# Optimization experiments

Measured on AMD Instinct MI355X. Metric: run time of the kernel, lower is better.

The kernel has to match this reference:

```python
import jax, jax.numpy as jnp
import numpy as np

B, S, D, H, FF = 4, 1024, 1024, 16, 4096
DH = D // H
EPS = 1e-5  # torch LayerNorm default


def _layernorm(x, g, b):
    m = jnp.mean(x, axis=-1, keepdims=True)
    v = jnp.mean((x - m) ** 2, axis=-1, keepdims=True)
    return (x - m) * jax.lax.rsqrt(v + EPS) * g + b


def setup_inputs() -> dict:
    key = jax.random.key(0)
    ks = jax.random.split(key, 8)
    init = lambda k, shape: jax.random.normal(k, shape, jnp.float32) * 0.02
    return {
        "x": jax.random.normal(ks[0], (B, S, D), jnp.float32),
        "Wq": init(ks[1], (D, D)), "bq": jnp.zeros((D,), jnp.float32),
        "Wk": init(ks[2], (D, D)), "bk": jnp.zeros((D,), jnp.float32),
        "Wv": init(ks[3], (D, D)), "bv": jnp.zeros((D,), jnp.float32),
        "Wo": init(ks[4], (D, D)), "bo": jnp.zeros((D,), jnp.float32),
        "ln1_g": jnp.ones((D,), jnp.float32), "ln1_b": jnp.zeros((D,), jnp.float32),
        "W1": init(ks[5], (D, FF)), "b1": jnp.zeros((FF,), jnp.float32),
        "W2": init(ks[6], (FF, D)), "b2": jnp.zeros((D,), jnp.float32),
        "ln2_g": jnp.ones((D,), jnp.float32), "ln2_b": jnp.zeros((D,), jnp.float32),
    }


def reference(x, Wq, bq, Wk, bk, Wv, bv, Wo, bo,
              ln1_g, ln1_b, W1, b1, W2, b2, ln2_g, ln2_b):
    Bx, Sx, _ = x.shape

    def heads(w, b):  # [B,S,D] -> [B,H,S,DH]
        return (x @ w + b).reshape(Bx, Sx, H, DH).transpose(0, 2, 1, 3)

    q, k, v = heads(Wq, bq), heads(Wk, bk), heads(Wv, bv)
    scores = jnp.einsum('bhqd,bhkd->bhqk', q, k) / jnp.sqrt(jnp.float32(DH))
    causal = jnp.tril(jnp.ones((Sx, Sx), bool))
    scores = jnp.where(causal[None, None], scores, jnp.float32(-1e9))
    attn = jax.nn.softmax(scores, axis=-1)           # [B,H,S,S]
    ctx = jnp.einsum('bhqk,bhkd->bqhd', attn, v).reshape(Bx, Sx, D)
    attn_out = ctx @ Wo + bo
    h = _layernorm(x + attn_out, ln1_g, ln1_b)
    ff = jax.nn.relu(h @ W1 + b1) @ W2 + b2
    y = _layernorm(h + ff, ln2_g, ln2_b)
    return (y, attn)
```

## Files before the change

kernel.cpp:

```cpp
#include <hip/hip_runtime.h>
#include <cstdint>


#define T_B 4
#define T_S 1024
#define T_D 1024
#define T_H 16
#define T_DH 64
#define T_FF 4096
#define T_TOK (T_B * T_S)

typedef __attribute__((ext_vector_type(8))) short bf16x8;
typedef __attribute__((ext_vector_type(4))) float f32x4;

__device__ __forceinline__ short f2bf(float f) {
  uint32_t u = __float_as_uint(f);
  u += 0x7FFFu + ((u >> 16) & 1u);
  return (short)(u >> 16);
}

__device__ __forceinline__ void async_copy16(void* lds, const void* g) {
  __builtin_amdgcn_global_load_lds(
      (__attribute__((address_space(1))) uint32_t*)(uintptr_t)g,
      (__attribute__((address_space(3))) uint32_t*)(uint32_t)(uintptr_t)lds,
      16, 0, 0);
}

__device__ __forceinline__ void mfma_loop_128x128(
    const short* __restrict__ A, int lda, const short* __restrict__ Bm, int ldb,
    int kLen, int m0, int n0, short* As, short* Bs, f32x4 acc[4][4]) {
  const int t = threadIdx.x;
  const int lane = t & 63, wid = t >> 6;
  const int wm = (wid >> 1) << 6, wn = (wid & 1) << 6;
  const int quad = lane >> 4, r16 = lane & 15;
  const int row0 = t >> 2;
  const int cb0 = (t & 3) << 4;

  const f32x4 zf = {0.f, 0.f, 0.f, 0.f};
#pragma unroll
  for (int i = 0; i < 4; ++i)
#pragma unroll
    for (int j = 0; j < 4; ++j) acc[i][j] = zf;

  for (int k0 = 0; k0 < kLen; k0 += 32) {
    __syncthreads();
    async_copy16((char*)As + (wid << 10),
                 (const char*)A + (((size_t)(m0 + row0) * lda + k0) << 1) + cb0);
    async_copy16((char*)As + 4096 + (wid << 10),
                 (const char*)A + (((size_t)(m0 + 64 + row0) * lda + k0) << 1) + cb0);
    async_copy16((char*)Bs + (wid << 10),
                 (const char*)Bm + (((size_t)(n0 + row0) * ldb + k0) << 1) + cb0);
    async_copy16((char*)Bs + 4096 + (wid << 10),
                 (const char*)Bm + (((size_t)(n0 + 64 + row0) * ldb + k0) << 1) + cb0);
    __syncthreads();
    bf16x8 av[4], bv[4];
#pragma unroll
    for (int i = 0; i < 4; ++i) {
      av[i] = *(const bf16x8*)(As + ((wm + i * 16 + r16) << 5) + (quad << 3));
      bv[i] = *(const bf16x8*)(Bs + ((wn + i * 16 + r16) << 5) + (quad << 3));
    }
#pragma unroll
    for (int mi = 0; mi < 4; ++mi)
#pragma unroll
      for (int ni = 0; ni < 4; ++ni)
        acc[mi][ni] = __builtin_amdgcn_mfma_f32_16x16x32_bf16(
            av[mi], bv[ni], acc[mi][ni], 0, 0, 0);
  }
}

template <int MODE>
__global__ __launch_bounds__(256) void gemm_dense(
    const short* __restrict__ A, const short* __restrict__ Bw, int K, int N,
    const float* __restrict__ bias0, const float* __restrict__ bias1,
    const float* __restrict__ bias2, short* __restrict__ outb0,
    short* __restrict__ outb1, short* __restrict__ outb2) {
  __shared__ __align__(16) short As[128 * 32];
  __shared__ __align__(16) short Bs[128 * 32];
  const int m0 = blockIdx.x << 7, n0 = blockIdx.y << 7;
  f32x4 acc[4][4];
  mfma_loop_128x128(A, K, Bw, K, K, m0, n0, As, Bs, acc);

  const int t = threadIdx.x;
  const int lane = t & 63, wid = t >> 6;
  const int wm = (wid >> 1) << 6, wn = (wid & 1) << 6;
  const int quad = lane >> 4, r16 = lane & 15;

  if constexpr (MODE == 0) {
    const int which = n0 >> 10;
    const float* bias = (which == 0) ? bias0 : (which == 1) ? bias1 : bias2;
#pragma unroll
    for (int mi = 0; mi < 4; ++mi) {
#pragma unroll
      for (int ni = 0; ni < 4; ++ni) {
        const int col = n0 + wn + ni * 16 + r16;
        const int c10 = col & 1023;
        const float bb = bias[c10];
        const int hh = c10 >> 6, dh = col & 63;
#pragma unroll
        for (int reg = 0; reg < 4; ++reg) {
          const int row = m0 + wm + mi * 16 + quad * 4 + reg;
          const int b = row >> 10, s = row & 1023;
          const short v = f2bf(acc[mi][ni][reg] + bb);
          if (which == 0)
            outb0[((((size_t)b * T_H + hh) * T_S) + s) * T_DH + dh] = v;
          else if (which == 1)
            outb1[((((size_t)b * T_H + hh) * T_S) + s) * T_DH + dh] = v;
          else
            outb2[(((size_t)b * T_H + hh) * T_DH + dh) * T_S + s] = v;
        }
      }
    }
  } else {
#pragma unroll
    for (int mi = 0; mi < 4; ++mi)
#pragma unroll
      for (int ni = 0; ni < 4; ++ni) {
        const int col = n0 + wn + ni * 16 + r16;
        const float bb = bias0[col];
#pragma unroll
        for (int reg = 0; reg < 4; ++reg) {
          const int row = m0 + wm + mi * 16 + quad * 4 + reg;
          outb0[(size_t)row * N + col] = f2bf(fmaxf(acc[mi][ni][reg] + bb, 0.f));
        }
      }
  }
}

__global__ __launch_bounds__(256) void gemm_splitk(
    const short* __restrict__ A, const short* __restrict__ Bw, int K, int N,
    int kc, float* __restrict__ outp) {
  __shared__ __align__(16) short As[128 * 32];
  __shared__ __align__(16) short Bs[128 * 32];
  const int m0 = blockIdx.x << 7, n0 = blockIdx.y << 7, z = blockIdx.z;
  f32x4 acc[4][4];
  mfma_loop_128x128(A + (size_t)z * kc, K, Bw + (size_t)z * kc, K, kc, m0, n0,
                    As, Bs, acc);
  float* o = outp + (size_t)z * T_TOK * N;
  const int t = threadIdx.x;
  const int lane = t & 63, wid = t >> 6;
  const int wm = (wid >> 1) << 6, wn = (wid & 1) << 6;
  const int quad = lane >> 4, r16 = lane & 15;
#pragma unroll
  for (int mi = 0; mi < 4; ++mi)
#pragma unroll
    for (int ni = 0; ni < 4; ++ni) {
      const int col = n0 + wn + ni * 16 + r16;
#pragma unroll
      for (int reg = 0; reg < 4; ++reg) {
        const int row = m0 + wm + mi * 16 + quad * 4 + reg;
        o[(size_t)row * N + col] = acc[mi][ni][reg];
      }
    }
}

__global__ __launch_bounds__(256) void attn_pass1(
    const short* __restrict__ qg, const short* __restrict__ kg,
    const short* __restrict__ vg, short* __restrict__ ctx,
    float* __restrict__ rsinv_g) {
  const int qb = blockIdx.x;
  const int bh = blockIdx.y;
  const int b = bh >> 4, h = bh & 15;
  const int m0 = qb << 7;
  __shared__ __align__(16) short Es[4 * 128 * 32];
  __shared__ float rsbuf[2][128];
  const int t = threadIdx.x;
  const int lane = t & 63, wid = t >> 6;
  const int quad = lane >> 4, r16 = lane & 15;
  const int wm = (wid >> 1) << 6, wn = (wid & 1) << 6;
  const int pvm = wid << 5;

  const short* Qbh = qg + (size_t)bh * T_S * T_DH;
  const short* Kbh = kg + (size_t)bh * T_S * T_DH;
  const short* Vbh = vg + (size_t)bh * T_DH * T_S;

  bf16x8 qf[4][2];
#pragma unroll
  for (int mi = 0; mi < 4; ++mi)
#pragma unroll
    for (int ksd = 0; ksd < 2; ++ksd)
      qf[mi][ksd] = *(const bf16x8*)(Qbh + (size_t)(m0 + wm + mi * 16 + r16) * T_DH +
                                     ksd * 32 + quad * 8);

  float rs[4][4];
#pragma unroll
  for (int i = 0; i < 4; ++i)
#pragma unroll
    for (int j = 0; j < 4; ++j) rs[i][j] = 0.f;
  const f32x4 zf = {0.f, 0.f, 0.f, 0.f};
  f32x4 accp[2][4];
#pragma unroll
  for (int i = 0; i < 2; ++i)
#pragma unroll
    for (int j = 0; j < 4; ++j) accp[i][j] = zf;

  for (int kt = 0; kt <= qb; ++kt) {
    f32x4 accs[4][4];
#pragma unroll
    for (int i = 0; i < 4; ++i)
#pragma unroll
      for (int j = 0; j < 4; ++j) accs[i][j] = zf;
#pragma unroll
    for (int ksd = 0; ksd < 2; ++ksd) {
      bf16x8 bv[4];
#pragma unroll
      for (int ni = 0; ni < 4; ++ni)
        bv[ni] = *(const bf16x8*)(Kbh + (size_t)(kt * 128 + wn + ni * 16 + r16) * T_DH +
                                  ksd * 32 + quad * 8);
#pragma unroll
      for (int mi = 0; mi < 4; ++mi)
#pragma unroll
        for (int ni = 0; ni < 4; ++ni)
          accs[mi][ni] = __builtin_amdgcn_mfma_f32_16x16x32_bf16(
              qf[mi][ksd], bv[ni], accs[mi][ni], 0, 0, 0);
    }
    __syncthreads();
    const bool diag = (kt == qb);
#pragma unroll
    for (int mi = 0; mi < 4; ++mi) {
#pragma unroll
      for (int ni = 0; ni < 4; ++ni) {
        const int cbase = wn + ni * 16;
        const int kse = cbase >> 5;
        const int sin = (cbase & 31) + r16;
        short* ep = Es + kse * 4096 + (wm + mi * 16 + quad * 4) * 32 + sin;
        const int colw = cbase + r16;
#pragma unroll
        for (int reg = 0; reg < 4; ++reg) {
          float e = __expf(accs[mi][ni][reg] * 0.125f);
          if (diag && colw > (wm + mi * 16 + quad * 4 + reg)) e = 0.f;
          ep[reg * 32] = f2bf(e);
          rs[mi][reg] += e;
        }
      }
    }
    __syncthreads();
#pragma unroll
    for (int ks = 0; ks < 4; ++ks) {
      bf16x8 av[2], bvv[4];
#pragma unroll
      for (int i = 0; i < 2; ++i)
        av[i] = *(const bf16x8*)(Es + ks * 4096 + (pvm + i * 16 + r16) * 32 + quad * 8);
#pragma unroll
      for (int ni = 0; ni < 4; ++ni)
        bvv[ni] = *(const bf16x8*)(Vbh + (size_t)(ni * 16 + r16) * T_S + kt * 128 +
                                   ks * 32 + quad * 8);
#pragma unroll
      for (int i = 0; i < 2; ++i)
#pragma unroll
        for (int ni = 0; ni < 4; ++ni)
          accp[i][ni] = __builtin_amdgcn_mfma_f32_16x16x32_bf16(av[i], bvv[ni],
                                                                accp[i][ni], 0, 0, 0);
    }
  }

#pragma unroll
  for (int mi = 0; mi < 4; ++mi)
#pragma unroll
    for (int reg = 0; reg < 4; ++reg) {
#pragma unroll
      for (int d = 1; d < 16; d <<= 1)
        rs[mi][reg] += __shfl_xor(rs[mi][reg], d, 64);
    }
  if (r16 == 0) {
#pragma unroll
    for (int mi = 0; mi < 4; ++mi)
#pragma unroll
      for (int reg = 0; reg < 4; ++reg)
        rsbuf[wid & 1][wm + mi * 16 + quad * 4 + reg] = rs[mi][reg];
  }
  __syncthreads();
  if (t < 128) {
    const float iv = 1.f / (rsbuf[0][t] + rsbuf[1][t]);
    rsbuf[0][t] = iv;
    rsinv_g[(size_t)bh * T_S + m0 + t] = iv;
  }
  __syncthreads();
#pragma unroll
  for (int i = 0; i < 2; ++i)
#pragma unroll
    for (int ni = 0; ni < 4; ++ni) {
#pragma unroll
      for (int reg = 0; reg < 4; ++reg) {
        const int row = pvm + i * 16 + quad * 4 + reg;
        const float iv = rsbuf[0][row];
        ctx[((size_t)b * T_S + m0 + row) * T_D + h * 64 + ni * 16 + r16] =
            f2bf(accp[i][ni][reg] * iv);
      }
    }
}

__global__ __launch_bounds__(256) void attn_pass2(
    const short* __restrict__ qg, const short* __restrict__ kg,
    const float* __restrict__ rsinv_g, float* __restrict__ attn) {
  const int qb = blockIdx.x, kt = blockIdx.y, bh = blockIdx.z;
  float* out = attn + ((size_t)bh * T_S + qb * 128) * T_S + kt * 128;
  const int t = threadIdx.x;
  if (kt > qb) {
    const float4 z4 = {0.f, 0.f, 0.f, 0.f};
#pragma unroll
    for (int j = 0; j < 16; ++j) {
      const int id = t + j * 256;
      ((float4*)(out + (size_t)(id >> 5) * T_S))[id & 31] = z4;
    }
    return;
  }
  const int lane = t & 63, wid = t >> 6;
  const int quad = lane >> 4, r16 = lane & 15;
  const int wm = (wid >> 1) << 6, wn = (wid & 1) << 6;
  const short* Qbh = qg + (size_t)bh * T_S * T_DH;
  const short* Kbh = kg + (size_t)bh * T_S * T_DH;
  const f32x4 zf = {0.f, 0.f, 0.f, 0.f};
  f32x4 accs[4][4];
#pragma unroll
  for (int i = 0; i < 4; ++i)
#pragma unroll
    for (int j = 0; j < 4; ++j) accs[i][j] = zf;
#pragma unroll
  for (int ksd = 0; ksd < 2; ++ksd) {
    bf16x8 aq[4], bv[4];
#pragma unroll
    for (int mi = 0; mi < 4; ++mi)
      aq[mi] = *(const bf16x8*)(Qbh + (size_t)(qb * 128 + wm + mi * 16 + r16) * T_DH +
                                ksd * 32 + quad * 8);
#pragma unroll
    for (int ni = 0; ni < 4; ++ni)
      bv[ni] = *(const bf16x8*)(Kbh + (size_t)(kt * 128 + wn + ni * 16 + r16) * T_DH +
                                ksd * 32 + quad * 8);
#pragma unroll
    for (int mi = 0; mi < 4; ++mi)
#pragma unroll
      for (int ni = 0; ni < 4; ++ni)
        accs[mi][ni] = __builtin_amdgcn_mfma_f32_16x16x32_bf16(aq[mi], bv[ni],
                                                               accs[mi][ni], 0, 0, 0);
  }
  const bool diag = (kt == qb);
#pragma unroll
  for (int mi = 0; mi < 4; ++mi)
#pragma unroll
    for (int ni = 0; ni < 4; ++ni) {
      const int col = wn + ni * 16 + r16;
#pragma unroll
      for (int reg = 0; reg < 4; ++reg) {
        const int rowt = wm + mi * 16 + quad * 4 + reg;
        const float iv = rsinv_g[(size_t)bh * T_S + qb * 128 + rowt];
        float e = __expf(accs[mi][ni][reg] * 0.125f) * iv;
        if (diag && col > rowt) e = 0.f;
        out[(size_t)rowt * T_S + col] = e;
      }
    }
}

__global__ __launch_bounds__(256) void ln_multi(
    const float* __restrict__ a, const float* __restrict__ parts, int nparts,
    const float* __restrict__ bias, const float* __restrict__ g,
    const float* __restrict__ be, float* __restrict__ outf,
    short* __restrict__ outb) {
  const int row = blockIdx.x;
  const int t = threadIdx.x;
  float4 x = ((const float4*)(a + (size_t)row * T_D))[t];
  const float4 bv = ((const float4*)bias)[t];
  x.x += bv.x; x.y += bv.y; x.z += bv.z; x.w += bv.w;
  for (int p = 0; p < nparts; ++p) {
    const float4 v = ((const float4*)(parts + (size_t)p * T_TOK * T_D + (size_t)row * T_D))[t];
    x.x += v.x; x.y += v.y; x.z += v.z; x.w += v.w;
  }
  float sum = x.x + x.y + x.z + x.w;
  float sq = x.x * x.x + x.y * x.y + x.z * x.z + x.w * x.w;
  __shared__ float reds[4], redq[4];
  const int lane = t & 63, wid = t >> 6;
#pragma unroll
  for (int o = 32; o > 0; o >>= 1) {
    sum += __shfl_down(sum, o, 64);
    sq += __shfl_down(sq, o, 64);
  }
  if (lane == 0) { reds[wid] = sum; redq[wid] = sq; }
  __syncthreads();
  sum = reds[0] + reds[1] + reds[2] + reds[3];
  sq = redq[0] + redq[1] + redq[2] + redq[3];
  const float mean = sum * (1.f / T_D);
  const float var = sq * (1.f / T_D) - mean * mean;
  const float rstd = rsqrtf(var + 1e-5f);
  const float4 gg = ((const float4*)g)[t];
  const float4 bb = ((const float4*)be)[t];
  float4 y;
  y.x = (x.x - mean) * rstd * gg.x + bb.x;
  y.y = (x.y - mean) * rstd * gg.y + bb.y;
  y.z = (x.z - mean) * rstd * gg.z + bb.z;
  y.w = (x.w - mean) * rstd * gg.w + bb.w;
  ((float4*)(outf + (size_t)row * T_D))[t] = y;
  if (outb != nullptr) {
    short4 o4;
    o4.x = f2bf(y.x); o4.y = f2bf(y.y); o4.z = f2bf(y.z); o4.w = f2bf(y.w);
    ((short4*)(outb + (size_t)row * T_D))[t] = o4;
  }
}

__global__ __launch_bounds__(256) void cvt_f32_bf16(const float* __restrict__ src,
                                                    short* __restrict__ dst) {
  const int i = blockIdx.x * 256 + threadIdx.x;
  const float4 v = ((const float4*)src)[i];
  short4 o;
  o.x = f2bf(v.x); o.y = f2bf(v.y); o.z = f2bf(v.z); o.w = f2bf(v.w);
  ((short4*)dst)[i] = o;
}

__global__ __launch_bounds__(1024) void transpose_cvt(const float* __restrict__ src,
                                                      short* __restrict__ dst,
                                                      int R, int C) {
  __shared__ float tile[32][33];
  const int c0 = blockIdx.x << 5, r0 = blockIdx.y << 5;
  tile[threadIdx.y][threadIdx.x] =
      src[(size_t)(r0 + threadIdx.y) * C + c0 + threadIdx.x];
  __syncthreads();
  dst[(size_t)(c0 + threadIdx.y) * R + r0 + threadIdx.x] =
      f2bf(tile[threadIdx.x][threadIdx.y]);
}

extern "C" void kernel_launch(void* const* d_in, const int* in_sizes, int n_in,
                              void* d_out, int out_size, void* d_ws,
                              size_t ws_size, hipStream_t stream) {
  const float* x = (const float*)d_in[0];
  const float* Wq = (const float*)d_in[1];
  const float* bq = (const float*)d_in[2];
  const float* Wk = (const float*)d_in[3];
  const float* bk = (const float*)d_in[4];
  const float* Wv = (const float*)d_in[5];
  const float* bv = (const float*)d_in[6];
  const float* Wo = (const float*)d_in[7];
  const float* bo = (const float*)d_in[8];
  const float* ln1g = (const float*)d_in[9];
  const float* ln1b = (const float*)d_in[10];
  const float* W1 = (const float*)d_in[11];
  const float* b1 = (const float*)d_in[12];
  const float* W2 = (const float*)d_in[13];
  const float* b2 = (const float*)d_in[14];
  const float* ln2g = (const float*)d_in[15];
  const float* ln2b = (const float*)d_in[16];
  (void)in_sizes; (void)n_in; (void)out_size; (void)ws_size;

  float* y_out = (float*)d_out;
  float* attn = (float*)d_out + (size_t)T_TOK * T_D;

  char* w = (char*)d_ws;
  size_t off = 0;
  auto alloc = [&](size_t bytes) -> void* {
    void* p = w + off;
    off += (bytes + 255) & ~(size_t)255;
    return p;
  };
  short* xb     = (short*)alloc((size_t)T_TOK * T_D * 2);
  short* Wqkv_t = (short*)alloc((size_t)3 * T_D * T_D * 2);
  short* Wo_t   = (short*)alloc((size_t)T_D * T_D * 2);
  short* W1_t   = (short*)alloc((size_t)T_FF * T_D * 2);
  short* W2_t   = (short*)alloc((size_t)T_D * T_FF * 2);
  short* qb_    = (short*)alloc((size_t)T_TOK * T_D * 2);
  short* kb_    = (short*)alloc((size_t)T_TOK * T_D * 2);
  short* vtb    = (short*)alloc((size_t)T_TOK * T_D * 2);
  short* ctx    = (short*)alloc((size_t)T_TOK * T_D * 2);
  short* hb     = (short*)alloc((size_t)T_TOK * T_D * 2);
  short* ff1    = (short*)alloc((size_t)T_TOK * T_FF * 2);
  float* hf     = (float*)alloc((size_t)T_TOK * T_D * 4);
  float* rsinv  = (float*)alloc((size_t)T_H * T_B * T_S * 4);
  float* woP    = (float*)alloc((size_t)2 * T_TOK * T_D * 4);
  float* ffP    = (float*)alloc((size_t)4 * T_TOK * T_D * 4);

  cvt_f32_bf16<<<dim3(4096), dim3(256), 0, stream>>>(x, xb);
  transpose_cvt<<<dim3(32, 32), dim3(32, 32), 0, stream>>>(Wq, Wqkv_t, T_D, T_D);
  transpose_cvt<<<dim3(32, 32), dim3(32, 32), 0, stream>>>(Wk, Wqkv_t + T_D * T_D, T_D, T_D);
  transpose_cvt<<<dim3(32, 32), dim3(32, 32), 0, stream>>>(Wv, Wqkv_t + 2 * T_D * T_D, T_D, T_D);
  transpose_cvt<<<dim3(32, 32), dim3(32, 32), 0, stream>>>(Wo, Wo_t, T_D, T_D);
  transpose_cvt<<<dim3(128, 32), dim3(32, 32), 0, stream>>>(W1, W1_t, T_D, T_FF);
  transpose_cvt<<<dim3(32, 128), dim3(32, 32), 0, stream>>>(W2, W2_t, T_FF, T_D);

  gemm_dense<0><<<dim3(32, 24), dim3(256), 0, stream>>>(
      xb, Wqkv_t, T_D, 3072, bq, bk, bv, qb_, kb_, vtb);
  attn_pass1<<<dim3(8, 64), dim3(256), 0, stream>>>(qb_, kb_, vtb, ctx, rsinv);
  attn_pass2<<<dim3(8, 8, 64), dim3(256), 0, stream>>>(qb_, kb_, rsinv, attn);
  gemm_splitk<<<dim3(32, 8, 2), dim3(256), 0, stream>>>(ctx, Wo_t, T_D, T_D, 512, woP);
  ln_multi<<<dim3(4096), dim3(256), 0, stream>>>(x, woP, 2, bo, ln1g, ln1b, hf, hb);
  gemm_dense<2><<<dim3(32, 32), dim3(256), 0, stream>>>(
      hb, W1_t, T_D, T_FF, b1, nullptr, nullptr, ff1, nullptr, nullptr);
  gemm_splitk<<<dim3(32, 8, 4), dim3(256), 0, stream>>>(ff1, W2_t, T_FF, T_D, 1024, ffP);
  ln_multi<<<dim3(4096), dim3(256), 0, stream>>>(hf, ffP, 4, b2, ln2g, ln2b, y_out, nullptr);
}
```

Before: 670.0 us.

## Use BK=64 GEMM tiles, LDS-staged V transpose, merged prep kernel, bf16 residual

```diff
diff --git a/kernel.cpp b/kernel.cpp
--- a/kernel.cpp
+++ b/kernel.cpp
@@ -19,6 +19,10 @@
   return (short)(u >> 16);
 }
 
+__device__ __forceinline__ float bf2f(short s) {
+  return __uint_as_float(((uint32_t)(unsigned short)s) << 16);
+}
+
 __device__ __forceinline__ void async_copy16(void* lds, const void* g) {
   __builtin_amdgcn_global_load_lds(
       (__attribute__((address_space(1))) uint32_t*)(uintptr_t)g,
@@ -26,45 +30,59 @@
       16, 0, 0);
 }
 
-__device__ __forceinline__ void mfma_loop_128x128(
+__device__ __forceinline__ void stage32(short* dstA, short* dstB,
+                                        const short* A, int lda, const short* Bm,
+                                        int ldb, int m0, int n0, int k0, int t,
+                                        int wid) {
+  const int row0 = t >> 2;
+  const int cb0 = (t & 3) << 4;
+  async_copy16((char*)dstA + (wid << 10),
+               (const char*)A + (((size_t)(m0 + row0) * lda + k0) << 1) + cb0);
+  async_copy16((char*)dstA + 4096 + (wid << 10),
+               (const char*)A + (((size_t)(m0 + 64 + row0) * lda + k0) << 1) + cb0);
+  async_copy16((char*)dstB + (wid << 10),
+               (const char*)Bm + (((size_t)(n0 + row0) * ldb + k0) << 1) + cb0);
+  async_copy16((char*)dstB + 4096 + (wid << 10),
+               (const char*)Bm + (((size_t)(n0 + 64 + row0) * ldb + k0) << 1) + cb0);
+}
+
+__device__ __forceinline__ void compute32(const short* As, const short* Bs,
+                                          int wm, int wn, int quad, int r16,
+                                          f32x4 acc[4][4]) {
+  bf16x8 av[4], bv[4];
+#pragma unroll
+  for (int i = 0; i < 4; ++i) {
+    av[i] = *(const bf16x8*)(As + ((wm + i * 16 + r16) << 5) + (quad << 3));
+    bv[i] = *(const bf16x8*)(Bs + ((wn + i * 16 + r16) << 5) + (quad << 3));
+  }
+#pragma unroll
+  for (int mi = 0; mi < 4; ++mi)
+#pragma unroll
+    for (int ni = 0; ni < 4; ++ni)
+      acc[mi][ni] = __builtin_amdgcn_mfma_f32_16x16x32_bf16(av[mi], bv[ni],
+                                                            acc[mi][ni], 0, 0, 0);
+}
+
+__device__ __forceinline__ void mfma_loop_bk64(
     const short* __restrict__ A, int lda, const short* __restrict__ Bm, int ldb,
-    int kLen, int m0, int n0, short* As, short* Bs, f32x4 acc[4][4]) {
+    int kLen, int m0, int n0, short* As, short* As2, short* Bs, short* Bs2,
+    f32x4 acc[4][4]) {
   const int t = threadIdx.x;
   const int lane = t & 63, wid = t >> 6;
   const int wm = (wid >> 1) << 6, wn = (wid & 1) << 6;
   const int quad = lane >> 4, r16 = lane & 15;
-  const int row0 = t >> 2;
-  const int cb0 = (t & 3) << 4;
-
   const f32x4 zf = {0.f, 0.f, 0.f, 0.f};
 #pragma unroll
   for (int i = 0; i < 4; ++i)
 #pragma unroll
     for (int j = 0; j < 4; ++j) acc[i][j] = zf;
-
-  for (int k0 = 0; k0 < kLen; k0 += 32) {
+  for (int k0 = 0; k0 < kLen; k0 += 64) {
     __syncthreads();
-    async_copy16((char*)As + (wid << 10),
-                 (const char*)A + (((size_t)(m0 + row0) * lda + k0) << 1) + cb0);
-    async_copy16((char*)As + 4096 + (wid << 10),
-                 (const char*)A + (((size_t)(m0 + 64 + row0) * lda + k0) << 1) + cb0);
-    async_copy16((char*)Bs + (wid << 10),
-                 (const char*)Bm + (((size_t)(n0 + row0) * ldb + k0) << 1) + cb0);
-    async_copy16((char*)Bs + 4096 + (wid << 10),
-                 (const char*)Bm + (((size_t)(n0 + 64 + row0) * ldb + k0) << 1) + cb0);
+    stage32(As, Bs, A, lda, Bm, ldb, m0, n0, k0, t, wid);
+    stage32(As2, Bs2, A, lda, Bm, ldb, m0, n0, k0 + 32, t, wid);
     __syncthreads();
-    bf16x8 av[4], bv[4];
-#pragma unroll
-    for (int i = 0; i < 4; ++i) {
-      av[i] = *(const bf16x8*)(As + ((wm + i * 16 + r16) << 5) + (quad << 3));
-      bv[i] = *(const bf16x8*)(Bs + ((wn + i * 16 + r16) << 5) + (quad << 3));
-    }
-#pragma unroll
-    for (int mi = 0; mi < 4; ++mi)
-#pragma unroll
-      for (int ni = 0; ni < 4; ++ni)
-        acc[mi][ni] = __builtin_amdgcn_mfma_f32_16x16x32_bf16(
-            av[mi], bv[ni], acc[mi][ni], 0, 0, 0);
+    compute32(As, Bs, wm, wn, quad, r16, acc);
+    compute32(As2, Bs2, wm, wn, quad, r16, acc);
   }
 }
 
@@ -74,11 +92,14 @@
     const float* __restrict__ bias0, const float* __restrict__ bias1,
     const float* __restrict__ bias2, short* __restrict__ outb0,
     short* __restrict__ outb1, short* __restrict__ outb2) {
-  __shared__ __align__(16) short As[128 * 32];
-  __shared__ __align__(16) short Bs[128 * 32];
+  __shared__ __align__(16) char smem[MODE == 0 ? 34816 : 32768];
+  short* As = (short*)smem;
+  short* As2 = As + 4096;
+  short* Bs = As + 8192;
+  short* Bs2 = As + 12288;
   const int m0 = blockIdx.x << 7, n0 = blockIdx.y << 7;
   f32x4 acc[4][4];
-  mfma_loop_128x128(A, K, Bw, K, K, m0, n0, As, Bs, acc);
+  mfma_loop_bk64(A, K, Bw, K, K, m0, n0, As, As2, Bs, Bs2, acc);
 
   const int t = threadIdx.x;
   const int lane = t & 63, wid = t >> 6;
@@ -88,27 +109,50 @@
   if constexpr (MODE == 0) {
     const int which = n0 >> 10;
     const float* bias = (which == 0) ? bias0 : (which == 1) ? bias1 : bias2;
-#pragma unroll
-    for (int mi = 0; mi < 4; ++mi) {
-#pragma unroll
-      for (int ni = 0; ni < 4; ++ni) {
-        const int col = n0 + wn + ni * 16 + r16;
-        const int c10 = col & 1023;
-        const float bb = bias[c10];
-        const int hh = c10 >> 6, dh = col & 63;
-#pragma unroll
-        for (int reg = 0; reg < 4; ++reg) {
-          const int row = m0 + wm + mi * 16 + quad * 4 + reg;
-          const int b = row >> 10, s = row & 1023;
-          const short v = f2bf(acc[mi][ni][reg] + bb);
-          if (which == 0)
-            outb0[((((size_t)b * T_H + hh) * T_S) + s) * T_DH + dh] = v;
-          else if (which == 1)
-            outb1[((((size_t)b * T_H + hh) * T_S) + s) * T_DH + dh] = v;
-          else
-            outb2[(((size_t)b * T_H + hh) * T_DH + dh) * T_S + s] = v;
+    if (which < 2) {
+      short* outp = (which == 0) ? outb0 : outb1;
+#pragma unroll
+      for (int mi = 0; mi < 4; ++mi) {
+#pragma unroll
+        for (int ni = 0; ni < 4; ++ni) {
+          const int col = n0 + wn + ni * 16 + r16;
+          const int c10 = col & 1023;
+          const float bb = bias[c10];
+          const int hh = c10 >> 6, dh = col & 63;
+#pragma unroll
+          for (int reg = 0; reg < 4; ++reg) {
+            const int row = m0 + wm + mi * 16 + quad * 4 + reg;
+            const int b = row >> 10, s = row & 1023;
+            outp[((((size_t)b * T_H + hh) * T_S) + s) * T_DH + dh] =
+                f2bf(acc[mi][ni][reg] + bb);
+          }
         }
       }
+    } else {
+      __syncthreads();
+      short* vtile = (short*)smem;
+#pragma unroll
+      for (int mi = 0; mi < 4; ++mi)
+#pragma unroll
+        for (int ni = 0; ni < 4; ++ni) {
+          const int c = wn + ni * 16 + r16;
+          const float bb = bias[(n0 + c) & 1023];
+#pragma unroll
+          for (int reg = 0; reg < 4; ++reg) {
+            const int r = wm + mi * 16 + quad * 4 + reg;
+            vtile[c * 136 + r] = f2bf(acc[mi][ni][reg] + bb);
+          }
+        }
+      __syncthreads();
+      const int b = m0 >> 10, s0 = m0 & 1023;
+      const int c = t >> 1, half = t & 1;
+      const int c10 = (n0 + c) & 1023;
+      const int hh = c10 >> 6, dh = c10 & 63;
+      short* dst = outb2 + (((size_t)b * T_H + hh) * T_DH + dh) * T_S + s0 + half * 64;
+      const short* srcl = vtile + c * 136 + half * 64;
+#pragma unroll
+      for (int j = 0; j < 8; ++j)
+        *(bf16x8*)(dst + j * 8) = *(const bf16x8*)(srcl + j * 8);
     }
   } else {
 #pragma unroll
@@ -129,12 +173,15 @@
 __global__ __launch_bounds__(256) void gemm_splitk(
     const short* __restrict__ A, const short* __restrict__ Bw, int K, int N,
     int kc, float* __restrict__ outp) {
-  __shared__ __align__(16) short As[128 * 32];
-  __shared__ __align__(16) short Bs[128 * 32];
+  __shared__ __align__(16) char smem[32768];
+  short* As = (short*)smem;
+  short* As2 = As + 4096;
+  short* Bs = As + 8192;
+  short* Bs2 = As + 12288;
   const int m0 = blockIdx.x << 7, n0 = blockIdx.y << 7, z = blockIdx.z;
   f32x4 acc[4][4];
-  mfma_loop_128x128(A + (size_t)z * kc, K, Bw + (size_t)z * kc, K, kc, m0, n0,
-                    As, Bs, acc);
+  mfma_loop_bk64(A + (size_t)z * kc, K, Bw + (size_t)z * kc, K, kc, m0, n0, As,
+                 As2, Bs, Bs2, acc);
   float* o = outp + (size_t)z * T_TOK * N;
   const int t = threadIdx.x;
   const int lane = t & 63, wid = t >> 6;
@@ -351,17 +398,24 @@
 }
 
 __global__ __launch_bounds__(256) void ln_multi(
-    const float* __restrict__ a, const float* __restrict__ parts, int nparts,
-    const float* __restrict__ bias, const float* __restrict__ g,
-    const float* __restrict__ be, float* __restrict__ outf,
-    short* __restrict__ outb) {
+    const float* __restrict__ a32, const short* __restrict__ a16,
+    const float* __restrict__ parts, int nparts, const float* __restrict__ bias,
+    const float* __restrict__ g, const float* __restrict__ be,
+    float* __restrict__ outf, short* __restrict__ outb) {
   const int row = blockIdx.x;
   const int t = threadIdx.x;
-  float4 x = ((const float4*)(a + (size_t)row * T_D))[t];
+  float4 x;
+  if (a32 != nullptr) {
+    x = ((const float4*)(a32 + (size_t)row * T_D))[t];
+  } else {
+    const short4 s4 = ((const short4*)(a16 + (size_t)row * T_D))[t];
+    x.x = bf2f(s4.x); x.y = bf2f(s4.y); x.z = bf2f(s4.z); x.w = bf2f(s4.w);
+  }
   const float4 bv = ((const float4*)bias)[t];
   x.x += bv.x; x.y += bv.y; x.z += bv.z; x.w += bv.w;
   for (int p = 0; p < nparts; ++p) {
-    const float4 v = ((const float4*)(parts + (size_t)p * T_TOK * T_D + (size_t)row * T_D))[t];
+    const float4 v =
+        ((const float4*)(parts + (size_t)p * T_TOK * T_D + (size_t)row * T_D))[t];
     x.x += v.x; x.y += v.y; x.z += v.z; x.w += v.w;
   }
   float sum = x.x + x.y + x.z + x.w;
@@ -387,7 +441,7 @@
   y.y = (x.y - mean) * rstd * gg.y + bb.y;
   y.z = (x.z - mean) * rstd * gg.z + bb.z;
   y.w = (x.w - mean) * rstd * gg.w + bb.w;
-  ((float4*)(outf + (size_t)row * T_D))[t] = y;
+  if (outf != nullptr) ((float4*)(outf + (size_t)row * T_D))[t] = y;
   if (outb != nullptr) {
     short4 o4;
     o4.x = f2bf(y.x); o4.y = f2bf(y.y); o4.z = f2bf(y.z); o4.w = f2bf(y.w);
@@ -395,25 +449,44 @@
   }
 }
 
-__global__ __launch_bounds__(256) void cvt_f32_bf16(const float* __restrict__ src,
-                                                    short* __restrict__ dst) {
-  const int i = blockIdx.x * 256 + threadIdx.x;
-  const float4 v = ((const float4*)src)[i];
-  short4 o;
-  o.x = f2bf(v.x); o.y = f2bf(v.y); o.z = f2bf(v.z); o.w = f2bf(v.w);
-  ((short4*)dst)[i] = o;
-}
-
-__global__ __launch_bounds__(1024) void transpose_cvt(const float* __restrict__ src,
-                                                      short* __restrict__ dst,
-                                                      int R, int C) {
+__global__ __launch_bounds__(256) void prep_kernel(
+    const float* __restrict__ x, short* __restrict__ xb,
+    const float* __restrict__ Wq, const float* __restrict__ Wk,
+    const float* __restrict__ Wv, const float* __restrict__ Wo,
+    const float* __restrict__ W1, const float* __restrict__ W2,
+    short* __restrict__ Wqkv_t, short* __restrict__ Wo_t,
+    short* __restrict__ W1_t, short* __restrict__ W2_t) {
+  int id = blockIdx.x;
+  const int t = threadIdx.x;
+  if (id < 4096) {
+    const int i = id * 256 + t;
+    const float4 v = ((const float4*)x)[i];
+    short4 o;
+    o.x = f2bf(v.x); o.y = f2bf(v.y); o.z = f2bf(v.z); o.w = f2bf(v.w);
+    ((short4*)xb)[i] = o;
+    return;
+  }
+  id -= 4096;
+  const float* src;
+  short* dst;
+  int R, C;
+  if (id < 1024) { src = Wq; dst = Wqkv_t; R = 1024; C = 1024; }
+  else if (id < 2048) { id -= 1024; src = Wk; dst = Wqkv_t + 1024 * 1024; R = 1024; C = 1024; }
+  else if (id < 3072) { id -= 2048; src = Wv; dst = Wqkv_t + 2 * 1024 * 1024; R = 1024; C = 1024; }
+  else if (id < 4096) { id -= 3072; src = Wo; dst = Wo_t; R = 1024; C = 1024; }
+  else if (id < 8192) { id -= 4096; src = W1; dst = W1_t; R = 1024; C = 4096; }
+  else { id -= 8192; src = W2; dst = W2_t; R = 4096; C = 1024; }
+  const int tilesC = C >> 5;
+  const int r0 = (id / tilesC) << 5, c0 = (id % tilesC) << 5;
   __shared__ float tile[32][33];
-  const int c0 = blockIdx.x << 5, r0 = blockIdx.y << 5;
-  tile[threadIdx.y][threadIdx.x] =
-      src[(size_t)(r0 + threadIdx.y) * C + c0 + threadIdx.x];
+  const int tx = t & 31, ty = t >> 5;
+#pragma unroll
+  for (int j = 0; j < 4; ++j)
+    tile[ty + j * 8][tx] = src[(size_t)(r0 + ty + j * 8) * C + c0 + tx];
   __syncthreads();
-  dst[(size_t)(c0 + threadIdx.y) * R + r0 + threadIdx.x] =
-      f2bf(tile[threadIdx.x][threadIdx.y]);
+#pragma unroll
+  for (int j = 0; j < 4; ++j)
+    dst[(size_t)(c0 + ty + j * 8) * R + r0 + tx] = f2bf(tile[tx][ty + j * 8]);
 }
 
 extern "C" void kernel_launch(void* const* d_in, const int* in_sizes, int n_in,
@@ -459,27 +532,25 @@
   short* ctx    = (short*)alloc((size_t)T_TOK * T_D * 2);
   short* hb     = (short*)alloc((size_t)T_TOK * T_D * 2);
   short* ff1    = (short*)alloc((size_t)T_TOK * T_FF * 2);
-  float* hf     = (float*)alloc((size_t)T_TOK * T_D * 4);
   float* rsinv  = (float*)alloc((size_t)T_H * T_B * T_S * 4);
   float* woP    = (float*)alloc((size_t)2 * T_TOK * T_D * 4);
-  float* ffP    = (float*)alloc((size_t)4 * T_TOK * T_D * 4);
-
-  cvt_f32_bf16<<<dim3(4096), dim3(256), 0, stream>>>(x, xb);
-  transpose_cvt<<<dim3(32, 32), dim3(32, 32), 0, stream>>>(Wq, Wqkv_t, T_D, T_D);
-  transpose_cvt<<<dim3(32, 32), dim3(32, 32), 0, stream>>>(Wk, Wqkv_t + T_D * T_D, T_D, T_D);
-  transpose_cvt<<<dim3(32, 32), dim3(32, 32), 0, stream>>>(Wv, Wqkv_t + 2 * T_D * T_D, T_D, T_D);
-  transpose_cvt<<<dim3(32, 32), dim3(32, 32), 0, stream>>>(Wo, Wo_t, T_D, T_D);
-  transpose_cvt<<<dim3(128, 32), dim3(32, 32), 0, stream>>>(W1, W1_t, T_D, T_FF);
-  transpose_cvt<<<dim3(32, 128), dim3(32, 32), 0, stream>>>(W2, W2_t, T_FF, T_D);
+  float* ffP    = (float*)alloc((size_t)2 * T_TOK * T_D * 4);
+
+  prep_kernel<<<dim3(16384), dim3(256), 0, stream>>>(
+      x, xb, Wq, Wk, Wv, Wo, W1, W2, Wqkv_t, Wo_t, W1_t, W2_t);
 
   gemm_dense<0><<<dim3(32, 24), dim3(256), 0, stream>>>(
       xb, Wqkv_t, T_D, 3072, bq, bk, bv, qb_, kb_, vtb);
   attn_pass1<<<dim3(8, 64), dim3(256), 0, stream>>>(qb_, kb_, vtb, ctx, rsinv);
   attn_pass2<<<dim3(8, 8, 64), dim3(256), 0, stream>>>(qb_, kb_, rsinv, attn);
+
   gemm_splitk<<<dim3(32, 8, 2), dim3(256), 0, stream>>>(ctx, Wo_t, T_D, T_D, 512, woP);
-  ln_multi<<<dim3(4096), dim3(256), 0, stream>>>(x, woP, 2, bo, ln1g, ln1b, hf, hb);
+  ln_multi<<<dim3(4096), dim3(256), 0, stream>>>(x, nullptr, woP, 2, bo, ln1g,
+                                                 ln1b, nullptr, hb);
+
   gemm_dense<2><<<dim3(32, 32), dim3(256), 0, stream>>>(
       hb, W1_t, T_D, T_FF, b1, nullptr, nullptr, ff1, nullptr, nullptr);
-  gemm_splitk<<<dim3(32, 8, 4), dim3(256), 0, stream>>>(ff1, W2_t, T_FF, T_D, 1024, ffP);
-  ln_multi<<<dim3(4096), dim3(256), 0, stream>>>(hf, ffP, 4, b2, ln2g, ln2b, y_out, nullptr);
-}
+  gemm_splitk<<<dim3(32, 8, 2), dim3(256), 0, stream>>>(ff1, W2_t, T_FF, T_D, 2048, ffP);
+  ln_multi<<<dim3(4096), dim3(256), 0, stream>>>(nullptr, hb, ffP, 2, b2, ln2g,
+                                                 ln2b, y_out, nullptr);
+}
```

Measured after the change: 643.6 us. 3.9% less time.
